# Optimization experiments

Measured on AMD Instinct MI355X. Metric: run time of the kernel, lower is better.

## Reference

```python
import jax, jax.numpy as jnp
import numpy as np

S, B, I, H, O = 512, 64, 256, 1024, 128

def setup_inputs() -> dict:
    key = jax.random.key(0)
    ks = jax.random.split(key, 9)
    std0 = 1.0 / np.sqrt(H)
    inp = {
        "x": jax.random.normal(ks[0], (S, B, I), dtype=jnp.float32),
        "W_r0": jax.random.normal(ks[1], (H, I + H), dtype=jnp.float32) * std0,
        "b_r0": jnp.zeros((H,), jnp.float32),
        "W_z0": jax.random.normal(ks[2], (H, I + H), dtype=jnp.float32) * std0,
        "b_z0": jnp.zeros((H,), jnp.float32),
        "W_h0": jax.random.normal(ks[3], (H, I + H), dtype=jnp.float32) * std0,
        "b_h0": jnp.zeros((H,), jnp.float32),
        "W_r1": jax.random.normal(ks[4], (H, H + H), dtype=jnp.float32) * std0,
        "b_r1": jnp.zeros((H,), jnp.float32),
        "W_z1": jax.random.normal(ks[5], (H, H + H), dtype=jnp.float32) * std0,
        "b_z1": jnp.zeros((H,), jnp.float32),
        "W_h1": jax.random.normal(ks[6], (H, H + H), dtype=jnp.float32) * std0,
        "b_h1": jnp.zeros((H,), jnp.float32),
        "W_out": jax.random.normal(ks[7], (O, H), dtype=jnp.float32) * (1.0 / np.sqrt(H)),
        "b_out": jax.random.normal(ks[8], (O,), dtype=jnp.float32) * (1.0 / np.sqrt(H)),
    }
    return inp

def _gru_cell(x, h, W_r, b_r, W_z, b_z, W_h, b_h):
    # x: [B, in], h: [B, H]
    comb = jnp.concatenate([x, h], axis=1)
    r = jax.nn.sigmoid(comb @ W_r.T + b_r)
    z = jax.nn.sigmoid(comb @ W_z.T + b_z)
    rc = jnp.concatenate([x, r * h], axis=1)
    h_tilde = jnp.tanh(rc @ W_h.T + b_h)
    return (1.0 - z) * h + z * h_tilde

def reference(x, W_r0, b_r0, W_z0, b_z0, W_h0, b_h0,
              W_r1, b_r1, W_z1, b_z1, W_h1, b_h1, W_out, b_out):
    batch = x.shape[1]
    h0_init = jnp.zeros((batch, H), x.dtype)
    h1_init = jnp.zeros((batch, H), x.dtype)

    def step(carry, x_t):
        h0, h1 = carry
        h0 = _gru_cell(x_t, h0, W_r0, b_r0, W_z0, b_z0, W_h0, b_h0)
        h1 = _gru_cell(h0, h1, W_r1, b_r1, W_z1, b_z1, W_h1, b_h1)
        out_t = h1 @ W_out.T + b_out  # [B, O]
        return (h0, h1), out_t

    (h0_f, h1_f), outputs = jax.lax.scan(step, (h0_init, h1_init), x)
    return outputs, jnp.stack([h0_f, h1_f], axis=0)  # [S,B,O], [L,B,H]
```

## Files before the change

kernel.cpp:

```cpp
#include <hip/hip_runtime.h>

#define SLEN 512
#define BATCH 64
#define IDIM 256
#define HDIM 1024
#define ODIM 128
#define NBLK 256
#define NTHR 512
#define AGENT __HIP_MEMORY_SCOPE_AGENT
#define SLOTB 1605632ull

typedef unsigned short ushortT;
typedef unsigned long long ull;
typedef __attribute__((ext_vector_type(8))) short short8;
typedef __attribute__((ext_vector_type(4))) float f32x4;

__device__ __forceinline__ ushortT f2bf(float f) {
  unsigned u = __float_as_uint(f);
  unsigned r = (u + 0x7FFFu + ((u >> 16) & 1u)) >> 16;
  return (ushortT)r;
}

__device__ __forceinline__ void pack2(const float* __restrict__ s, ushortT* d) {
  float4 a = *(const float4*)s;
  float4 b = *(const float4*)(s + 16);
  short8 v;
  v[0]=(short)f2bf(a.x); v[1]=(short)f2bf(a.y); v[2]=(short)f2bf(a.z); v[3]=(short)f2bf(a.w);
  v[4]=(short)f2bf(b.x); v[5]=(short)f2bf(b.y); v[6]=(short)f2bf(b.z); v[7]=(short)f2bf(b.w);
  *(short8*)d = v;
}

__device__ __forceinline__ void pack2a(const float* __restrict__ s, ushortT* d) {
  float4 a = *(const float4*)s;
  float4 b = *(const float4*)(s + 16);
  ull lo = (ull)f2bf(a.x) | ((ull)f2bf(a.y) << 16) | ((ull)f2bf(a.z) << 32) | ((ull)f2bf(a.w) << 48);
  ull hi = (ull)f2bf(b.x) | ((ull)f2bf(b.y) << 16) | ((ull)f2bf(b.z) << 32) | ((ull)f2bf(b.w) << 48);
  __hip_atomic_store((ull*)d, lo, __ATOMIC_RELAXED, AGENT);
  __hip_atomic_store((ull*)(d + 4), hi, __ATOMIC_RELAXED, AGENT);
}

__device__ __forceinline__ void mir_store(ushortT* M, int row, int cL, float v) {
  int kt = cL >> 5, c5 = cL & 31;
  int h = c5 >> 4, g = (c5 >> 2) & 3, j = c5 & 3;
  int u = ((kt * 4 + (row >> 4)) * 64) + 16 * g + (row & 15);
  __hip_atomic_store(&M[(size_t)u * 8 + h * 4 + j], f2bf(v), __ATOMIC_RELAXED, AGENT);
}

__device__ __forceinline__ void st_f32x4(float* p, float v0, float v1, float v2, float v3) {
  ull lo = (ull)__float_as_uint(v0) | ((ull)__float_as_uint(v1) << 32);
  ull hi = (ull)__float_as_uint(v2) | ((ull)__float_as_uint(v3) << 32);
  __hip_atomic_store((ull*)p, lo, __ATOMIC_RELAXED, AGENT);
  __hip_atomic_store((ull*)(p + 2), hi, __ATOMIC_RELAXED, AGENT);
}

__device__ __forceinline__ void arrive(unsigned* sy, int blk, int tid, unsigned idx) {
  __syncthreads();
  if (tid == 0)
    __hip_atomic_store(&sy[16 * blk], idx, __ATOMIC_RELAXED, AGENT);
}

__device__ __forceinline__ void wait2(unsigned* sy, int tid,
                                      int b0, int n0, unsigned t0,
                                      int b1, int n1, unsigned t1,
                                      bool acq, int blk) {
  int s = -1; unsigned tg = 0;
  if (tid < n0) { s = b0 + tid; tg = t0; }
  else if (tid < n0 + n1) { s = b1 + (tid - n0); tg = t1; }
  if (s >= 0)
    while (__hip_atomic_load(&sy[16 * s], __ATOMIC_RELAXED, AGENT) < tg)
      __builtin_amdgcn_s_sleep(1);
  __syncthreads();
  if (acq) {
    if (tid == 0) __hip_atomic_load(&sy[16 * blk], __ATOMIC_ACQUIRE, AGENT);
    __syncthreads();
  }
}

template<int NKT, int SPLIT, int NC>
__device__ __forceinline__ f32x4 stage_mm16(
    const ushortT* __restrict__ mA, const ushortT* __restrict__ mB,
    const ushortT* WL, float (*red)[64][4], int l, int w)
{
  const int mt = w & 3, kh = w >> 2;
  constexpr int H = NKT / 2;
  const int lo = kh * H;
  const int g = l >> 4, col = l & 15;
  f32x4 acc = {0.f, 0.f, 0.f, 0.f};
  short8 af[H];
  #pragma unroll
  for (int t = 0; t < H; ++t) {
    const int kt = lo + t;
    const ushortT* p = (kt < SPLIT)
        ? mA + (size_t)((kt * 4 + mt) * 64 + l) * 8
        : mB + (size_t)(((kt - SPLIT) * 4 + mt) * 64 + l) * 8;
    af[t] = *(const short8*)p;
  }
  #pragma unroll
  for (int t = 0; t < H; ++t) {
    short8 b = {0,0,0,0,0,0,0,0};
    if (col < NC)
      b = *(const short8*)(&WL[(size_t)(((lo + t) * 4 + g) * NC + col) * 8]);
    acc = __builtin_amdgcn_mfma_f32_16x16x32_bf16(af[t], b, acc, 0, 0, 0);
  }
  if (w >= 4) *(f32x4*)&red[w - 4][l][0] = acc;
  __syncthreads();
  if (w < 4) { f32x4 o = *(f32x4*)&red[w][l][0]; acc += o; }
  return acc;
}

__device__ __forceinline__ float fold8(float v) {
  v += __shfl_xor(v, 8);
  v += __shfl_xor(v, 16);
  v += __shfl_xor(v, 32);
  return v;
}

__device__ __forceinline__ void out_dot(const ushortT* __restrict__ Mh1p,
                                        const ushortT* WLo, float bo,
                                        float* __restrict__ out,
                                        int s_store, int jo, int tid) {
  const int l = tid & 63, w = tid >> 6;
  const int rr = (w << 3) + (l & 7);
  const int ks = l >> 3;
  const int mt = rr >> 4, r15 = rr & 15;
  float a0 = 0.f;
  #pragma unroll
  for (int q = 0; q < 4; ++q) {
    const int kt = (ks << 2) + q;
    #pragma unroll
    for (int gg = 0; gg < 4; ++gg) {
      const int u = ((kt << 2) + mt) * 64 + (gg << 4) + r15;
      union { short8 v; ushortT us[8]; } M;
      M.v = *(const short8*)(Mh1p + (size_t)u * 8);
      ull wlo = *(const ull*)(WLo + kt * 36 + (gg << 2));
      ull whi = *(const ull*)(WLo + kt * 36 + 16 + (gg << 2));
      #pragma unroll
      for (int j = 0; j < 4; ++j) {
        float mv = __uint_as_float(((unsigned)M.us[j]) << 16);
        float wv = __uint_as_float((unsigned)((wlo >> (16 * j)) & 0xFFFFu) << 16);
        a0 = fmaf(mv, wv, a0);
      }
      #pragma unroll
      for (int j = 0; j < 4; ++j) {
        float mv = __uint_as_float(((unsigned)M.us[4 + j]) << 16);
        float wv = __uint_as_float((unsigned)((whi >> (16 * j)) & 0xFFFFu) << 16);
        a0 = fmaf(mv, wv, a0);
      }
    }
  }
  float v = fold8(a0);
  if ((l & 56) == 0)
    out[((size_t)s_store * BATCH + rr) * ODIM + jo] = v + bo;
}

__global__ __launch_bounds__(NTHR, 2) void gru_pipe(
    const float* __restrict__ x,
    const float* __restrict__ Wr0, const float* __restrict__ br0,
    const float* __restrict__ Wz0, const float* __restrict__ bz0,
    const float* __restrict__ Wh0, const float* __restrict__ bh0,
    const float* __restrict__ Wr1, const float* __restrict__ br1,
    const float* __restrict__ Wz1, const float* __restrict__ bz1,
    const float* __restrict__ Wh1, const float* __restrict__ bh1,
    const float* __restrict__ Wout, const float* __restrict__ bout,
    float* __restrict__ out, char* __restrict__ ws, int nrot)
{
  __shared__ ushortT WSH[53248];
  __shared__ float red[4][64][4];

  const int blk = blockIdx.x;
  const int tid = threadIdx.x;
  const int l = tid & 63;
  const int w = tid >> 6;
  const int g = l >> 4;
  const int colL = l & 15;
  const int rowb = (w << 4) + (g << 2);

  unsigned* sy = (unsigned*)ws;
  char* slots = ws + 16384;

  ushortT* WA = WSH;
  ushortT* WB = WSH + (blk < 128 ? 20480 : 32768);

  if (blk < 128) {
    const int j0 = blk * 8;
    for (int u = tid; u < 40 * 4 * 16; u += NTHR) {
      int kt = u >> 6, gg = (u >> 4) & 3, c = u & 15;
      const float* src = (c < 8 ? Wr0 + (size_t)(j0 + c) * 1280
                                : Wz0 + (size_t)(j0 + c - 8) * 1280) + kt * 32 + gg * 4;
      pack2(src, &WA[(size_t)u * 8]);
    }
  } else {
    const int j1 = (blk - 128) * 8;
    for (int u = tid; u < 64 * 4 * 16; u += NTHR) {
      int kt = u >> 6, gg = (u >> 4) & 3, c = u & 15;
      const float* src = (c < 8 ? Wr1 + (size_t)(j1 + c) * 2048
                                : Wz1 + (size_t)(j1 + c - 8) * 2048) + kt * 32 + gg * 4;
      pack2(src, &WA[(size_t)u * 8]);
    }
  }
  if (blk < 64) {
    const int c0 = blk * 16;
    for (int u = tid; u < 40 * 4 * 16; u += NTHR) {
      int kt = u >> 6, gg = (u >> 4) & 3, c = u & 15;
      pack2(Wh0 + (size_t)(c0 + c) * 1280 + kt * 32 + gg * 4, &WB[(size_t)u * 8]);
    }
  } else if (blk < 128) {
    const int c0 = (blk - 64) * 16;
    for (int u = tid; u < 64 * 4 * 16; u += NTHR) {
      int kt = u >> 6, gg = (u >> 4) & 3, c = u & 15;
      pack2(Wh1 + (size_t)(c0 + c) * 2048 + kt * 32 + gg * 4, &WB[(size_t)u * 8]);
    }
  } else {
    for (int u = tid; u < 256; u += NTHR) {
      float4 a = *(const float4*)(Wout + (size_t)(blk - 128) * HDIM + (u << 2));
      int kt = u >> 3, c4 = (u & 7) << 2;
      ushortT* dst = &WB[kt * 36 + c4];
      dst[0] = f2bf(a.x); dst[1] = f2bf(a.y); dst[2] = f2bf(a.z); dst[3] = f2bf(a.w);
    }
  }
  if (blk >= 128 && tid < 16) {
    ushortT* Mx0 = (ushortT*)(slots + 1572864);
    int u = ((blk - 128) << 4) + tid;
    int kt = u >> 8, mtu = (u >> 6) & 3, lane = u & 63;
    int row = (mtu << 4) + (lane & 15), gg = lane >> 4;
    pack2a(x + (size_t)row * IDIM + (kt << 5) + (gg << 2), Mx0 + (size_t)u * 8);
  }

  float biasA = 0.f, biasB = 0.f, bo = 0.f;
  int cgA = 0, cgB = 0;
  if (blk < 128) {
    cgA = (blk << 3) + (colL & 7);
    biasA = (colL < 8) ? br0[cgA] : bz0[cgA];
  } else {
    cgA = ((blk - 128) << 3) + (colL & 7);
    biasA = (colL < 8) ? br1[cgA] : bz1[cgA];
  }
  if (blk < 64)       { cgB = (blk << 4) + colL;        biasB = bh0[cgB]; }
  else if (blk < 128) { cgB = ((blk - 64) << 4) + colL; biasB = bh1[cgB]; }
  else                { bo = bout[blk - 128]; }

  arrive(sy, blk, tid, 1u);
  wait2(sy, tid, 0, 256, 1u, 0, 0, 0u, true, blk);

  for (int i = 0; i <= SLEN; ++i) {
    const int pc = i % nrot;
    const int pp = (i + nrot - 1) % nrot;
    const int pn = (i + 1) % nrot;
    char* Spc = slots + SLOTB * pc;
    char* Spp = slots + SLOTB * pp;

    const float* h0prev = (const float*)Spp;
    float*       h0cur  = (float*)Spc;
    const float* h1prev = (const float*)(Spp + 262144);
    float*       h1cur  = (float*)(Spc + 262144);
    float* z0f = (float*)(Spc + 524288);
    float* z1f = (float*)(Spc + 786432);
    const ushortT* Mh0p = (const ushortT*)(Spp + 1048576);
    ushortT*       Mh0w = (ushortT*)(Spc + 1048576);
    const ushortT* Mh1p = (const ushortT*)(Spp + 1179648);
    ushortT*       Mh1w = (ushortT*)(Spc + 1179648);
    ushortT* Mrh0 = (ushortT*)(Spc + 1310720);
    ushortT* Mrh1 = (ushortT*)(Spc + 1441792);
    const ushortT* MxP = (const ushortT*)(Spc + 1572864);
    ushortT*       MxW = (ushortT*)(slots + SLOTB * pn + 1572864);

    const unsigned eA = 2u * (unsigned)i + 2u;
    const unsigned eB = 2u * (unsigned)i + 3u;
    const bool acqA = (i % nrot) == 0;
    const bool acqB = ((i + 1) % nrot) == 0 || i == SLEN;

    if (blk < 128) {
      if (i < SLEN) {
        float4 hq = {0.f, 0.f, 0.f, 0.f};
        if (w < 4 && colL < 8)
          hq = *(const float4*)(h0prev + (size_t)cgA * 64 + rowb);
        f32x4 acc = stage_mm16<40, 8, 16>(MxP, Mh0p, WA, red, l, w);
        if (w < 4) {
          float sg[4];
          #pragma unroll
          for (int r = 0; r < 4; ++r)
            sg[r] = 1.f / (1.f + __expf(-(acc[r] + biasA)));
          if (colL < 8) {
            mir_store(Mrh0, rowb + 0, cgA, sg[0] * hq.x);
            mir_store(Mrh0, rowb + 1, cgA, sg[1] * hq.y);
            mir_store(Mrh0, rowb + 2, cgA, sg[2] * hq.z);
            mir_store(Mrh0, rowb + 3, cgA, sg[3] * hq.w);
          } else {
            st_f32x4(z0f + (size_t)cgA * 64 + rowb, sg[0], sg[1], sg[2], sg[3]);
          }
        }
      }
    } else {
      if (i + 1 < SLEN && tid < 16) {
        int u = ((blk - 128) << 4) + tid;
        int kt = u >> 8, mtu = (u >> 6) & 3, lane = u & 63;
        int row = (mtu << 4) + (lane & 15), gg = lane >> 4;
        pack2a(x + ((size_t)(i + 1) * BATCH + row) * IDIM + (kt << 5) + (gg << 2),
               MxW + (size_t)u * 8);
      }
      if (i >= 1) {
        float4 hq = {0.f, 0.f, 0.f, 0.f};
        if (w < 4 && colL < 8)
          hq = *(const float4*)(h1prev + (size_t)cgA * 64 + rowb);
        f32x4 acc = stage_mm16<64, 32, 16>(Mh0p, Mh1p, WA, red, l, w);
        if (w < 4) {
          float sg[4];
          #pragma unroll
          for (int r = 0; r < 4; ++r)
            sg[r] = 1.f / (1.f + __expf(-(acc[r] + biasA)));
          if (colL < 8) {
            mir_store(Mrh1, rowb + 0, cgA, sg[0] * hq.x);
            mir_store(Mrh1, rowb + 1, cgA, sg[1] * hq.y);
            mir_store(Mrh1, rowb + 2, cgA, sg[2] * hq.z);
            mir_store(Mrh1, rowb + 3, cgA, sg[3] * hq.w);
          } else {
            st_f32x4(z1f + (size_t)cgA * 64 + rowb, sg[0], sg[1], sg[2], sg[3]);
          }
        }
      }
    }
    arrive(sy, blk, tid, eA);
    if (blk < 64)        wait2(sy, tid, 0, 128, eA, 0, 0, 0u, acqA, blk);
    else if (blk < 128)  wait2(sy, tid, 128, 128, eA, 0, 0, 0u, acqA, blk);
    else                 wait2(sy, tid, 0, 0, 0u, 0, 0, 0u, acqA, blk);

    if (blk < 64) {
      if (i < SLEN) {
        float4 zq = {0.f, 0.f, 0.f, 0.f}, hq = {0.f, 0.f, 0.f, 0.f};
        if (w < 4) {
          zq = *(const float4*)(z0f + (size_t)cgB * 64 + rowb);
          hq = *(const float4*)(h0prev + (size_t)cgB * 64 + rowb);
        }
        f32x4 acc = stage_mm16<40, 8, 16>(MxP, Mrh0, WB, red, l, w);
        if (w < 4) {
          float hn[4];
          const float hpv[4] = {hq.x, hq.y, hq.z, hq.w};
          const float zv[4] = {zq.x, zq.y, zq.z, zq.w};
          #pragma unroll
          for (int r = 0; r < 4; ++r) {
            float ht = tanhf(acc[r] + biasB);
            hn[r] = fmaf(zv[r], ht - hpv[r], hpv[r]);
            mir_store(Mh0w, rowb + r, cgB, hn[r]);
          }
          st_f32x4(h0cur + (size_t)cgB * 64 + rowb, hn[0], hn[1], hn[2], hn[3]);
        }
      }
    } else if (blk < 128) {
      if (i >= 1) {
        float4 zq = {0.f, 0.f, 0.f, 0.f}, hq = {0.f, 0.f, 0.f, 0.f};
        if (w < 4) {
          zq = *(const float4*)(z1f + (size_t)cgB * 64 + rowb);
          hq = *(const float4*)(h1prev + (size_t)cgB * 64 + rowb);
        }
        f32x4 acc = stage_mm16<64, 32, 16>(Mh0p, Mrh1, WB, red, l, w);
        if (w < 4) {
          float hn[4];
          const float hpv[4] = {hq.x, hq.y, hq.z, hq.w};
          const float zv[4] = {zq.x, zq.y, zq.z, zq.w};
          #pragma unroll
          for (int r = 0; r < 4; ++r) {
            float ht = tanhf(acc[r] + biasB);
            hn[r] = fmaf(zv[r], ht - hpv[r], hpv[r]);
            mir_store(Mh1w, rowb + r, cgB, hn[r]);
          }
          st_f32x4(h1cur + (size_t)cgB * 64 + rowb, hn[0], hn[1], hn[2], hn[3]);
        }
      }
    } else {
      if (i >= 2)
        out_dot(Mh1p, WB, bo, out, i - 2, blk - 128, tid);
    }
    arrive(sy, blk, tid, eB);
    if (blk < 128) wait2(sy, tid, 0, 64, eB, 128, 128, eA, acqB, blk);
    else           wait2(sy, tid, 0, 128, eB, 0, 0, 0u, acqB, blk);
  }

  wait2(sy, tid, 0, 256, 2u * (unsigned)SLEN + 3u, 0, 0, 0u, true, blk);
  {
    char* Sf1 = slots + SLOTB * (SLEN % nrot);
    char* Sf0 = slots + SLOTB * ((SLEN - 1) % nrot);
    if (blk >= 128)
      out_dot((const ushortT*)(Sf1 + 1179648), WB, bo, out, SLEN - 1, blk - 128, tid);
    const float* h0fin = (const float*)Sf0;
    const float* h1fin = (const float*)(Sf1 + 262144);
    const size_t base = (size_t)SLEN * BATCH * ODIM;
    const int u = blk * NTHR + tid;
    float v;
    if (u < 65536) {
      int row = u >> 10, col = u & 1023;
      v = h0fin[(size_t)col * 64 + row];
    } else {
      int t = u - 65536;
      int row = t >> 10, col = t & 1023;
      v = h1fin[(size_t)col * 64 + row];
    }
    out[base + u] = v;
  }
}

extern "C" void kernel_launch(void* const* d_in, const int* in_sizes, int n_in,
                              void* d_out, int out_size, void* d_ws, size_t ws_size,
                              hipStream_t stream) {
  const float* xx  = (const float*)d_in[0];
  const float* Wr0 = (const float*)d_in[1];
  const float* br0 = (const float*)d_in[2];
  const float* Wz0 = (const float*)d_in[3];
  const float* bz0 = (const float*)d_in[4];
  const float* Wh0 = (const float*)d_in[5];
  const float* bh0 = (const float*)d_in[6];
  const float* Wr1 = (const float*)d_in[7];
  const float* br1 = (const float*)d_in[8];
  const float* Wz1 = (const float*)d_in[9];
  const float* bz1 = (const float*)d_in[10];
  const float* Wh1 = (const float*)d_in[11];
  const float* bh1 = (const float*)d_in[12];
  const float* Wou = (const float*)d_in[13];
  const float* bou = (const float*)d_in[14];

  long long avail = (long long)ws_size - 16384;
  int nrot = (int)(avail / (long long)SLOTB);
  if (nrot > 16) nrot = 16;
  if (nrot < 2) nrot = 2;

  hipMemsetAsync(d_ws, 0, 16384 + (size_t)nrot * SLOTB, stream);

  gru_pipe<<<dim3(NBLK), dim3(NTHR), 0, stream>>>(
      xx, Wr0, br0, Wz0, bz0, Wh0, bh0,
      Wr1, br1, Wz1, bz1, Wh1, bh1, Wou, bou,
      (float*)d_out, (char*)d_ws, nrot);
}
```

Baseline: 6.631 ms.

## Rebalance GRU work across blocks and precompute layer-1 candidate input half early

Layer-0 r/z gates and the candidate now share a block group of 64 blocks, each computing 16 columns of both gates together. Blocks 64-127, which handle the layer-1 candidate, now compute the Wh1·h0 half during phase A and add it to the r*h1 half in phase B. This shortens the critical path of phase B and lets the layer-0 phase-A barrier wait on 64 blocks instead of 128. The cost is more shared memory per block and a different per-block work balance, and the minimum rotation count is raised to 4.

```diff
diff --git a/kernel.cpp b/kernel.cpp
--- a/kernel.cpp
+++ b/kernel.cpp
@@ -106,6 +106,46 @@
   __syncthreads();
   if (w < 4) { f32x4 o = *(f32x4*)&red[w][l][0]; acc += o; }
   return acc;
+}
+
+template<int NKT, int SPLIT>
+__device__ __forceinline__ void stage_gates(
+    const ushortT* __restrict__ mA, const ushortT* __restrict__ mB,
+    const ushortT* WL, float (*redR)[64][4], float (*redZ)[64][4],
+    int l, int w, f32x4& accR, f32x4& accZ)
+{
+  const int mt = w & 3, kh = w >> 2;
+  constexpr int H = NKT / 2;
+  const int lo = kh * H;
+  const int g = l >> 4, col = l & 15;
+  accR = (f32x4){0.f, 0.f, 0.f, 0.f};
+  accZ = (f32x4){0.f, 0.f, 0.f, 0.f};
+  short8 af[H];
+  #pragma unroll
+  for (int t = 0; t < H; ++t) {
+    const int kt = lo + t;
+    const ushortT* p = (kt < SPLIT)
+        ? mA + (size_t)((kt * 4 + mt) * 64 + l) * 8
+        : mB + (size_t)(((kt - SPLIT) * 4 + mt) * 64 + l) * 8;
+    af[t] = *(const short8*)p;
+  }
+  #pragma unroll
+  for (int t = 0; t < H; ++t) {
+    const int kt = lo + t;
+    short8 bR = *(const short8*)(&WL[(size_t)((kt * 4 + g) * 32 + col) * 8]);
+    short8 bZ = *(const short8*)(&WL[(size_t)((kt * 4 + g) * 32 + 16 + col) * 8]);
+    accR = __builtin_amdgcn_mfma_f32_16x16x32_bf16(af[t], bR, accR, 0, 0, 0);
+    accZ = __builtin_amdgcn_mfma_f32_16x16x32_bf16(af[t], bZ, accZ, 0, 0, 0);
+  }
+  if (w >= 4) {
+    *(f32x4*)&redR[w - 4][l][0] = accR;
+    *(f32x4*)&redZ[w - 4][l][0] = accZ;
+  }
+  __syncthreads();
+  if (w < 4) {
+    accR += *(f32x4*)&redR[w][l][0];
+    accZ += *(f32x4*)&redZ[w][l][0];
+  }
 }
 
 __device__ __forceinline__ float fold8(float v) {
@@ -164,8 +204,9 @@
     const float* __restrict__ Wout, const float* __restrict__ bout,
     float* __restrict__ out, char* __restrict__ ws, int nrot)
 {
-  __shared__ ushortT WSH[53248];
-  __shared__ float red[4][64][4];
+  __shared__ ushortT WSH[61440];
+  __shared__ float redA[4][64][4];
+  __shared__ float redB[4][64][4];
 
   const int blk = blockIdx.x;
   const int tid = threadIdx.x;
@@ -178,16 +219,24 @@
   unsigned* sy = (unsigned*)ws;
   char* slots = ws + 16384;
 
-  ushortT* WA = WSH;
-  ushortT* WB = WSH + (blk < 128 ? 20480 : 32768);
-
-  if (blk < 128) {
-    const int j0 = blk * 8;
+  if (blk < 64) {
+    const int cb = blk * 16;
+    for (int u = tid; u < 40 * 4 * 32; u += NTHR) {
+      int kt = u >> 7, gg = (u >> 5) & 3, c = u & 31;
+      const float* src = (c < 16 ? Wr0 + (size_t)(cb + c) * 1280
+                                 : Wz0 + (size_t)(cb + c - 16) * 1280) + kt * 32 + gg * 4;
+      pack2(src, &WSH[(size_t)u * 8]);
+    }
     for (int u = tid; u < 40 * 4 * 16; u += NTHR) {
       int kt = u >> 6, gg = (u >> 4) & 3, c = u & 15;
-      const float* src = (c < 8 ? Wr0 + (size_t)(j0 + c) * 1280
-                                : Wz0 + (size_t)(j0 + c - 8) * 1280) + kt * 32 + gg * 4;
-      pack2(src, &WA[(size_t)u * 8]);
+      pack2(Wh0 + (size_t)(cb + c) * 1280 + kt * 32 + gg * 4,
+            &WSH[40960 + (size_t)u * 8]);
+    }
+  } else if (blk < 128) {
+    const int cb = (blk - 64) * 16;
+    for (int u = tid; u < 64 * 4 * 16; u += NTHR) {
+      int kt = u >> 6, gg = (u >> 4) & 3, c = u & 15;
+      pack2(Wh1 + (size_t)(cb + c) * 2048 + kt * 32 + gg * 4, &WSH[(size_t)u * 8]);
     }
   } else {
     const int j1 = (blk - 128) * 8;
@@ -195,26 +244,12 @@
       int kt = u >> 6, gg = (u >> 4) & 3, c = u & 15;
       const float* src = (c < 8 ? Wr1 + (size_t)(j1 + c) * 2048
                                 : Wz1 + (size_t)(j1 + c - 8) * 2048) + kt * 32 + gg * 4;
-      pack2(src, &WA[(size_t)u * 8]);
-    }
-  }
-  if (blk < 64) {
-    const int c0 = blk * 16;
-    for (int u = tid; u < 40 * 4 * 16; u += NTHR) {
-      int kt = u >> 6, gg = (u >> 4) & 3, c = u & 15;
-      pack2(Wh0 + (size_t)(c0 + c) * 1280 + kt * 32 + gg * 4, &WB[(size_t)u * 8]);
-    }
-  } else if (blk < 128) {
-    const int c0 = (blk - 64) * 16;
-    for (int u = tid; u < 64 * 4 * 16; u += NTHR) {
-      int kt = u >> 6, gg = (u >> 4) & 3, c = u & 15;
-      pack2(Wh1 + (size_t)(c0 + c) * 2048 + kt * 32 + gg * 4, &WB[(size_t)u * 8]);
-    }
-  } else {
+      pack2(src, &WSH[(size_t)u * 8]);
+    }
     for (int u = tid; u < 256; u += NTHR) {
       float4 a = *(const float4*)(Wout + (size_t)(blk - 128) * HDIM + (u << 2));
       int kt = u >> 3, c4 = (u & 7) << 2;
-      ushortT* dst = &WB[kt * 36 + c4];
+      ushortT* dst = &WSH[32768 + kt * 36 + c4];
       dst[0] = f2bf(a.x); dst[1] = f2bf(a.y); dst[2] = f2bf(a.z); dst[3] = f2bf(a.w);
     }
   }
@@ -226,18 +261,20 @@
     pack2a(x + (size_t)row * IDIM + (kt << 5) + (gg << 2), Mx0 + (size_t)u * 8);
   }
 
-  float biasA = 0.f, biasB = 0.f, bo = 0.f;
+  float biasR = 0.f, biasZ = 0.f, biasA = 0.f, biasB = 0.f, bo = 0.f;
   int cgA = 0, cgB = 0;
-  if (blk < 128) {
-    cgA = (blk << 3) + (colL & 7);
-    biasA = (colL < 8) ? br0[cgA] : bz0[cgA];
+  if (blk < 64) {
+    cgA = blk * 16 + colL;
+    cgB = cgA;
+    biasR = br0[cgA]; biasZ = bz0[cgA]; biasB = bh0[cgB];
+  } else if (blk < 128) {
+    cgB = (blk - 64) * 16 + colL;
+    biasB = bh1[cgB];
   } else {
     cgA = ((blk - 128) << 3) + (colL & 7);
     biasA = (colL < 8) ? br1[cgA] : bz1[cgA];
-  }
-  if (blk < 64)       { cgB = (blk << 4) + colL;        biasB = bh0[cgB]; }
-  else if (blk < 128) { cgB = ((blk - 64) << 4) + colL; biasB = bh1[cgB]; }
-  else                { bo = bout[blk - 128]; }
+    bo = bout[blk - 128];
+  }
 
   arrive(sy, blk, tid, 1u);
   wait2(sy, tid, 0, 256, 1u, 0, 0, 0u, true, blk);
@@ -269,27 +306,31 @@
     const bool acqA = (i % nrot) == 0;
     const bool acqB = ((i + 1) % nrot) == 0 || i == SLEN;
 
-    if (blk < 128) {
+    f32x4 accP = {0.f, 0.f, 0.f, 0.f};
+
+    if (blk < 64) {
       if (i < SLEN) {
         float4 hq = {0.f, 0.f, 0.f, 0.f};
-        if (w < 4 && colL < 8)
-          hq = *(const float4*)(h0prev + (size_t)cgA * 64 + rowb);
-        f32x4 acc = stage_mm16<40, 8, 16>(MxP, Mh0p, WA, red, l, w);
-        if (w < 4) {
-          float sg[4];
+        if (w < 4) hq = *(const float4*)(h0prev + (size_t)cgA * 64 + rowb);
+        f32x4 aR, aZ;
+        stage_gates<40, 8>(MxP, Mh0p, WSH, redA, redB, l, w, aR, aZ);
+        if (w < 4) {
+          float sgR[4], sgZ[4];
           #pragma unroll
-          for (int r = 0; r < 4; ++r)
-            sg[r] = 1.f / (1.f + __expf(-(acc[r] + biasA)));
-          if (colL < 8) {
-            mir_store(Mrh0, rowb + 0, cgA, sg[0] * hq.x);
-            mir_store(Mrh0, rowb + 1, cgA, sg[1] * hq.y);
-            mir_store(Mrh0, rowb + 2, cgA, sg[2] * hq.z);
-            mir_store(Mrh0, rowb + 3, cgA, sg[3] * hq.w);
-          } else {
-            st_f32x4(z0f + (size_t)cgA * 64 + rowb, sg[0], sg[1], sg[2], sg[3]);
+          for (int r = 0; r < 4; ++r) {
+            sgR[r] = 1.f / (1.f + __expf(-(aR[r] + biasR)));
+            sgZ[r] = 1.f / (1.f + __expf(-(aZ[r] + biasZ)));
           }
-        }
-      }
+          mir_store(Mrh0, rowb + 0, cgA, sgR[0] * hq.x);
+          mir_store(Mrh0, rowb + 1, cgA, sgR[1] * hq.y);
+          mir_store(Mrh0, rowb + 2, cgA, sgR[2] * hq.z);
+          mir_store(Mrh0, rowb + 3, cgA, sgR[3] * hq.w);
+          st_f32x4(z0f + (size_t)cgA * 64 + rowb, sgZ[0], sgZ[1], sgZ[2], sgZ[3]);
+        }
+      }
+    } else if (blk < 128) {
+      if (i >= 1)
+        accP = stage_mm16<32, 32, 16>(Mh0p, Mh0p, WSH, redA, l, w);
     } else {
       if (i + 1 < SLEN && tid < 16) {
         int u = ((blk - 128) << 4) + tid;
@@ -302,7 +343,7 @@
         float4 hq = {0.f, 0.f, 0.f, 0.f};
         if (w < 4 && colL < 8)
           hq = *(const float4*)(h1prev + (size_t)cgA * 64 + rowb);
-        f32x4 acc = stage_mm16<64, 32, 16>(Mh0p, Mh1p, WA, red, l, w);
+        f32x4 acc = stage_mm16<64, 32, 16>(Mh0p, Mh1p, WSH, redA, l, w);
         if (w < 4) {
           float sg[4];
           #pragma unroll
@@ -320,7 +361,7 @@
       }
     }
     arrive(sy, blk, tid, eA);
-    if (blk < 64)        wait2(sy, tid, 0, 128, eA, 0, 0, 0u, acqA, blk);
+    if (blk < 64)        wait2(sy, tid, 0, 64, eA, 0, 0, 0u, acqA, blk);
     else if (blk < 128)  wait2(sy, tid, 128, 128, eA, 0, 0, 0u, acqA, blk);
     else                 wait2(sy, tid, 0, 0, 0u, 0, 0, 0u, acqA, blk);
 
@@ -331,7 +372,7 @@
           zq = *(const float4*)(z0f + (size_t)cgB * 64 + rowb);
           hq = *(const float4*)(h0prev + (size_t)cgB * 64 + rowb);
         }
-        f32x4 acc = stage_mm16<40, 8, 16>(MxP, Mrh0, WB, red, l, w);
+        f32x4 acc = stage_mm16<40, 8, 16>(MxP, Mrh0, WSH + 40960, redA, l, w);
         if (w < 4) {
           float hn[4];
           const float hpv[4] = {hq.x, hq.y, hq.z, hq.w};
@@ -352,8 +393,9 @@
           zq = *(const float4*)(z1f + (size_t)cgB * 64 + rowb);
           hq = *(const float4*)(h1prev + (size_t)cgB * 64 + rowb);
         }
-        f32x4 acc = stage_mm16<64, 32, 16>(Mh0p, Mrh1, WB, red, l, w);
-        if (w < 4) {
+        f32x4 acc = stage_mm16<32, 0, 16>(Mrh1, Mrh1, WSH + 16384, redA, l, w);
+        if (w < 4) {
+          acc += accP;
           float hn[4];
           const float hpv[4] = {hq.x, hq.y, hq.z, hq.w};
           const float zv[4] = {zq.x, zq.y, zq.z, zq.w};
@@ -368,11 +410,12 @@
       }
     } else {
       if (i >= 2)
-        out_dot(Mh1p, WB, bo, out, i - 2, blk - 128, tid);
+        out_dot(Mh1p, WSH + 32768, bo, out, i - 2, blk - 128, tid);
     }
     arrive(sy, blk, tid, eB);
-    if (blk < 128) wait2(sy, tid, 0, 64, eB, 128, 128, eA, acqB, blk);
-    else           wait2(sy, tid, 0, 128, eB, 0, 0, 0u, acqB, blk);
+    if (blk < 64)        wait2(sy, tid, 0, 64, eB, 128, 128, eA, acqB, blk);
+    else if (blk < 128)  wait2(sy, tid, 0, 64, eB, 0, 0, 0u, acqB, blk);
+    else                 wait2(sy, tid, 0, 128, eB, 0, 0, 0u, acqB, blk);
   }
 
   wait2(sy, tid, 0, 256, 2u * (unsigned)SLEN + 3u, 0, 0, 0u, true, blk);
@@ -380,7 +423,8 @@
     char* Sf1 = slots + SLOTB * (SLEN % nrot);
     char* Sf0 = slots + SLOTB * ((SLEN - 1) % nrot);
     if (blk >= 128)
-      out_dot((const ushortT*)(Sf1 + 1179648), WB, bo, out, SLEN - 1, blk - 128, tid);
+      out_dot((const ushortT*)(Sf1 + 1179648), WSH + 32768, bo, out,
+              SLEN - 1, blk - 128, tid);
     const float* h0fin = (const float*)Sf0;
     const float* h1fin = (const float*)(Sf1 + 262144);
     const size_t base = (size_t)SLEN * BATCH * ODIM;
@@ -420,7 +464,7 @@
   long long avail = (long long)ws_size - 16384;
   int nrot = (int)(avail / (long long)SLOTB);
   if (nrot > 16) nrot = 16;
-  if (nrot < 2) nrot = 2;
+  if (nrot < 4) nrot = 4;
 
   hipMemsetAsync(d_ws, 0, 16384 + (size_t)nrot * SLOTB, stream);
 
```

Result: slower. 11.18 ms (+68.7%).
